# Optimization experiments

Hardware: AMD Instinct MI355X
Metric: run time of the kernel (lower is better)

Reference implementation:

```python
import jax, jax.numpy as jnp
import numpy as np

B, H, W, C = 128, 14, 14, 768

def setup_inputs() -> dict:
    key = jax.random.key(0)
    k1, k2 = jax.random.split(key)
    x = jax.random.normal(k1, (B, H, W, C), dtype=jnp.float32)
    # nn.Parameter(torch.randn(h, w//2+1, dim, 2) * 0.02)
    complex_weight = jax.random.normal(k2, (H, W // 2 + 1, C, 2), dtype=jnp.float32) * 0.02
    return {"x": x, "complex_weight": complex_weight}

def reference(x, complex_weight):
    b, h, w, c = x.shape
    xf = jnp.fft.rfft2(x.astype(jnp.float32), axes=(1, 2), norm='ortho')  # [B,H,W//2+1,C] complex
    weight = jax.lax.complex(complex_weight[..., 0], complex_weight[..., 1])  # [h,w//2+1,c]
    xf = xf * weight  # broadcast over batch
    return jnp.fft.irfft2(xf, s=(h, w), axes=(1, 2), norm='ortho')
```

## Files before the change

kernel.cpp:

```cpp
#include <hip/hip_runtime.h>
#include <hip/hip_bf16.h>


typedef _Float16 h2 __attribute__((ext_vector_type(2)));

#define BATCH 128
#define CC 768
#define SPAT 196
#define CPB 64
#define TB 448

__global__ __launch_bounds__(896) void gf_build_kd(const float* __restrict__ wg,
                                                   unsigned int* __restrict__ kd) {
    __shared__ float ws[112 * 128];
    __shared__ float ct[14], st[14];
    int t = threadIdx.x;
    int c0 = blockIdx.x * 64;
    int m  = blockIdx.y;
    if (t < 14) {
        float ang = 6.283185307179586f * (float)t / 14.0f;
        ct[t] = cosf(ang);
        st[t] = sinf(ang);
    }
    #pragma unroll
    for (int j = 0; j < 16; ++j) {
        int f = t + j * 896;
        int uv = f >> 7;
        int v = uv & 7;
        float scale = (v == 0 || v == 7) ? (1.0f / 196.0f) : (2.0f / 196.0f);
        ws[f] = wg[(size_t)uv * 1536 + (size_t)c0 * 2 + (f & 127)] * scale;
    }
    __syncthreads();

    int q = t >> 6, cl = t & 63;
    int pe = 2 * m;
    int po = (pe + 13) % 14;
    float ae = 0.f, ao = 0.f;
    int upe = 0, upo = 0;
    #pragma unroll
    for (int u = 0; u < 14; ++u) {
        int vq = 0;
        #pragma unroll
        for (int v = 0; v < 8; ++v) {
            int re = upe + vq; if (re >= 14) re -= 14;
            int ro = upo + vq; if (ro >= 14) ro -= 14;
            float wr = ws[(u * 8 + v) * 128 + cl * 2];
            float wi = ws[(u * 8 + v) * 128 + cl * 2 + 1];
            ae += wr * ct[re]; ae -= wi * st[re];
            ao += wr * ct[ro]; ao -= wi * st[ro];
            vq += q; if (vq >= 14) vq -= 14;
        }
        upe += pe; if (upe >= 14) upe -= 14;
        upo += po; if (upo >= 14) upo -= 14;
    }
    h2 pk; pk.x = (_Float16)ae; pk.y = (_Float16)ao;
    kd[((size_t)m * 14 + q) * CC + c0 + cl] = __builtin_bit_cast(unsigned int, pk);
}

__global__ __launch_bounds__(TB, 4) void gf_conv(const float* __restrict__ x,
                                                 const unsigned int* __restrict__ kd,
                                                 float* __restrict__ y) {
    extern __shared__ unsigned int lds[];
    int b = blockIdx.y;
    int c0 = blockIdx.x * CPB;
    int t = threadIdx.x;
    const float* xb = x + (size_t)b * SPAT * CC + c0;

    #pragma unroll
    for (int j = 0; j < 14; ++j) {
        int e = t + j * TB;
        lds[12544 + e] = kd[(size_t)(e >> 6) * CC + c0 + (e & 63)];
    }
    #pragma unroll
    for (int j = 0; j < 14; ++j) {
        int e = t + j * TB;
        int i = e / 896;
        int rem = e - i * 896;
        int w_ = rem >> 6, cl_ = rem & 63;
        int r0 = 2 * i, r1 = 2 * i + 1;
        int r2 = (r1 + 1 == 14) ? 0 : r1 + 1;
        float a  = xb[((size_t)r0 * 14 + w_) * CC + cl_];
        float bb = xb[((size_t)r1 * 14 + w_) * CC + cl_];
        float c2 = xb[((size_t)r2 * 14 + w_) * CC + cl_];
        h2 pe_; pe_.x = (_Float16)a;  pe_.y = (_Float16)bb;
        h2 po_; po_.x = (_Float16)bb; po_.y = (_Float16)c2;
        lds[e]        = __builtin_bit_cast(unsigned int, pe_);
        lds[6272 + e] = __builtin_bit_cast(unsigned int, po_);
    }
    __syncthreads();

    int cl = t & 63, g = t >> 6;
    h2 acc0[14], acc1[14];
    #pragma unroll
    for (int w = 0; w < 14; ++w) {
        acc0[w] = (h2)(_Float16)0.0f;
        acc1[w] = (h2)(_Float16)0.0f;
    }

    int m = g;
    #pragma unroll
    for (int i = 0; i < 7; ++i) {
        h2 xev[14], xov[14];
        #pragma unroll
        for (int w = 0; w < 14; ++w) {
            xev[w] = __builtin_bit_cast(h2, lds[i * 896 + w * 64 + cl]);
            xov[w] = __builtin_bit_cast(h2, lds[6272 + i * 896 + w * 64 + cl]);
        }
        #pragma unroll
        for (int q = 0; q < 14; ++q) {
            h2 kq = __builtin_bit_cast(h2, lds[12544 + m * 896 + q * 64 + cl]);
            #pragma unroll
            for (int w = 0; w < 14; ++w) {
                int src = w - q; if (src < 0) src += 14;
                acc0[w] = kq * xev[src] + acc0[w];
                acc1[w] = kq * xov[src] + acc1[w];
            }
        }
        m = (m == 0) ? 6 : m - 1;
    }

    float* yb = y + (size_t)b * SPAT * CC + c0;
    int h0 = 2 * g;
    #pragma unroll
    for (int w = 0; w < 14; ++w) {
        yb[((size_t)h0 * 14 + w) * CC + cl]       = (float)acc0[w].x + (float)acc0[w].y;
        yb[((size_t)(h0 + 1) * 14 + w) * CC + cl] = (float)acc1[w].x + (float)acc1[w].y;
    }
}

extern "C" void kernel_launch(void* const* d_in, const int* in_sizes, int n_in,
                              void* d_out, int out_size, void* d_ws, size_t ws_size,
                              hipStream_t stream) {
    const float* x = (const float*)d_in[0];
    const float* w = (const float*)d_in[1];
    float* y = (float*)d_out;
    unsigned int* kbuf = (unsigned int*)d_ws;

    gf_build_kd<<<dim3(12, 7), dim3(896), 0, stream>>>(w, kbuf);

    dim3 grid(CC / CPB, BATCH);
    size_t lds_bytes = 3 * 6272 * sizeof(unsigned int);
    gf_conv<<<grid, dim3(TB), lds_bytes, stream>>>(x, kbuf, y);
}
```

Baseline: 105.8 us.

## Replace LDS-staged conv with register sliding window and split fp32/fp16 batches

Rewrites the circular-convolution kernel so each single-wave block handles one output row pair and streams input rows and kernel taps straight from global memory into a register window with prefetch, removing the LDS staging and barrier. Accumulation moves from packed fp16 to fp32, using fdot2 for half the batches and plain fp32 FMAs for the other half, launched as two separate kernels. This lowers fp16 accumulation error but raises ALU work on the fp32 half, re-reads input across row-group blocks, and gives small blocks with high register pressure.

```diff
diff --git a/kernel.cpp b/kernel.cpp
--- a/kernel.cpp
+++ b/kernel.cpp
@@ -6,9 +6,6 @@
 
 #define BATCH 128
 #define CC 768
-#define SPAT 196
-#define CPB 64
-#define TB 448
 
 __global__ __launch_bounds__(896) void gf_build_kd(const float* __restrict__ wg,
                                                    unsigned int* __restrict__ kd) {
@@ -57,74 +54,92 @@
     kd[((size_t)m * 14 + q) * CC + c0 + cl] = __builtin_bit_cast(unsigned int, pk);
 }
 
-__global__ __launch_bounds__(TB, 4) void gf_conv(const float* __restrict__ x,
-                                                 const unsigned int* __restrict__ kd,
-                                                 float* __restrict__ y) {
-    extern __shared__ unsigned int lds[];
-    int b = blockIdx.y;
-    int c0 = blockIdx.x * CPB;
-    int t = threadIdx.x;
-    const float* xb = x + (size_t)b * SPAT * CC + c0;
+template<bool USE_F16>
+__global__ __launch_bounds__(64, 2) void gf_conv_t(const float* __restrict__ x,
+                                                   const unsigned int* __restrict__ kd,
+                                                   float* __restrict__ y, int b_base) {
+    int b  = b_base + blockIdx.y;
+    int c0 = blockIdx.x * 64;
+    int cl = threadIdx.x;
+    int g  = blockIdx.z;
+    const float* xb = x + (size_t)b * 196 * CC + c0 + cl;
+    const unsigned int* kb = kd + c0 + cl;
+
+    float acc0[14], acc1[14];
+    #pragma unroll
+    for (int w = 0; w < 14; ++w) { acc0[w] = 0.f; acc1[w] = 0.f; }
+
+    float win[5][14];
+    unsigned int kq[2][14];
 
     #pragma unroll
-    for (int j = 0; j < 14; ++j) {
-        int e = t + j * TB;
-        lds[12544 + e] = kd[(size_t)(e >> 6) * CC + c0 + (e & 63)];
+    for (int w = 0; w < 14; ++w) {
+        win[0][w] = xb[(0 * 14 + w) * CC];
+        win[1][w] = xb[(1 * 14 + w) * CC];
+        win[2][w] = xb[(2 * 14 + w) * CC];
     }
-    #pragma unroll
-    for (int j = 0; j < 14; ++j) {
-        int e = t + j * TB;
-        int i = e / 896;
-        int rem = e - i * 896;
-        int w_ = rem >> 6, cl_ = rem & 63;
-        int r0 = 2 * i, r1 = 2 * i + 1;
-        int r2 = (r1 + 1 == 14) ? 0 : r1 + 1;
-        float a  = xb[((size_t)r0 * 14 + w_) * CC + cl_];
-        float bb = xb[((size_t)r1 * 14 + w_) * CC + cl_];
-        float c2 = xb[((size_t)r2 * 14 + w_) * CC + cl_];
-        h2 pe_; pe_.x = (_Float16)a;  pe_.y = (_Float16)bb;
-        h2 po_; po_.x = (_Float16)bb; po_.y = (_Float16)c2;
-        lds[e]        = __builtin_bit_cast(unsigned int, pe_);
-        lds[6272 + e] = __builtin_bit_cast(unsigned int, po_);
-    }
-    __syncthreads();
-
-    int cl = t & 63, g = t >> 6;
-    h2 acc0[14], acc1[14];
-    #pragma unroll
-    for (int w = 0; w < 14; ++w) {
-        acc0[w] = (h2)(_Float16)0.0f;
-        acc1[w] = (h2)(_Float16)0.0f;
+    {
+        int m = g;
+        #pragma unroll
+        for (int q = 0; q < 14; ++q) kq[0][q] = kb[(m * 14 + q) * CC];
     }
 
-    int m = g;
     #pragma unroll
     for (int i = 0; i < 7; ++i) {
-        h2 xev[14], xov[14];
-        #pragma unroll
-        for (int w = 0; w < 14; ++w) {
-            xev[w] = __builtin_bit_cast(h2, lds[i * 896 + w * 64 + cl]);
-            xov[w] = __builtin_bit_cast(h2, lds[6272 + i * 896 + w * 64 + cl]);
-        }
-        #pragma unroll
-        for (int q = 0; q < 14; ++q) {
-            h2 kq = __builtin_bit_cast(h2, lds[12544 + m * 896 + q * 64 + cl]);
+        if (i < 6) {
+            const int sA = (2 * i + 3) % 5, sB = (2 * i + 4) % 5;
+            const int rA = 2 * i + 3, rB = (2 * i + 4) % 14;
             #pragma unroll
             for (int w = 0; w < 14; ++w) {
-                int src = w - q; if (src < 0) src += 14;
-                acc0[w] = kq * xev[src] + acc0[w];
-                acc1[w] = kq * xov[src] + acc1[w];
+                win[sA][w] = xb[(rA * 14 + w) * CC];
+                win[sB][w] = xb[(rB * 14 + w) * CC];
+            }
+            int m = g - (i + 1); if (m < 0) m += 7;
+            #pragma unroll
+            for (int q = 0; q < 14; ++q) kq[(i + 1) & 1][q] = kb[(m * 14 + q) * CC];
+        }
+        const int s0 = (2 * i) % 5, s1 = (2 * i + 1) % 5, s2 = (2 * i + 2) % 5;
+
+        if constexpr (USE_F16) {
+            h2 xev[14], xov[14];
+            #pragma unroll
+            for (int w = 0; w < 14; ++w) {
+                xev[w] = __builtin_bit_cast(h2, __builtin_amdgcn_cvt_pkrtz(win[s0][w], win[s1][w]));
+                xov[w] = __builtin_bit_cast(h2, __builtin_amdgcn_cvt_pkrtz(win[s1][w], win[s2][w]));
+            }
+            #pragma unroll
+            for (int q = 0; q < 14; ++q) {
+                h2 kv = __builtin_bit_cast(h2, kq[i & 1][q]);
+                #pragma unroll
+                for (int w = 0; w < 14; ++w) {
+                    int src = w - q; if (src < 0) src += 14;
+                    acc0[w] = __builtin_amdgcn_fdot2(kv, xev[src], acc0[w], false);
+                    acc1[w] = __builtin_amdgcn_fdot2(kv, xov[src], acc1[w], false);
+                }
+            }
+        } else {
+            #pragma unroll
+            for (int q = 0; q < 14; ++q) {
+                h2 kv = __builtin_bit_cast(h2, kq[i & 1][q]);
+                float ke = (float)kv.x, ko = (float)kv.y;
+                #pragma unroll
+                for (int w = 0; w < 14; ++w) {
+                    int src = w - q; if (src < 0) src += 14;
+                    acc0[w] += ke * win[s0][src];
+                    acc0[w] += ko * win[s1][src];
+                    acc1[w] += ke * win[s1][src];
+                    acc1[w] += ko * win[s2][src];
+                }
             }
         }
-        m = (m == 0) ? 6 : m - 1;
     }
 
-    float* yb = y + (size_t)b * SPAT * CC + c0;
+    float* yb = y + (size_t)b * 196 * CC + c0 + cl;
     int h0 = 2 * g;
     #pragma unroll
     for (int w = 0; w < 14; ++w) {
-        yb[((size_t)h0 * 14 + w) * CC + cl]       = (float)acc0[w].x + (float)acc0[w].y;
-        yb[((size_t)(h0 + 1) * 14 + w) * CC + cl] = (float)acc1[w].x + (float)acc1[w].y;
+        yb[(h0 * 14 + w) * CC]       = acc0[w];
+        yb[((h0 + 1) * 14 + w) * CC] = acc1[w];
     }
 }
 
@@ -138,7 +153,7 @@
 
     gf_build_kd<<<dim3(12, 7), dim3(896), 0, stream>>>(w, kbuf);
 
-    dim3 grid(CC / CPB, BATCH);
-    size_t lds_bytes = 3 * 6272 * sizeof(unsigned int);
-    gf_conv<<<grid, dim3(TB), lds_bytes, stream>>>(x, kbuf, y);
+    dim3 grid(12, 64, 7);
+    gf_conv_t<false><<<grid, dim3(64), 0, stream>>>(x, kbuf, y, 0);
+    gf_conv_t<true ><<<grid, dim3(64), 0, stream>>>(x, kbuf, y, 64);
 }
```

Measured after the change: 172.9 us. 63.5% more time.
